# Kernel tuning notes

Measured on AMD Instinct MI355X. Metric: run time of the kernel, lower is better.

The kernel has to match this reference:

```python
import jax, jax.numpy as jnp
import numpy as np

B, S, H, NH = 2, 2048, 2048, 16
HD = H // NH


def setup_inputs() -> dict:
    key = jax.random.key(0)
    ks = jax.random.split(key, 9)
    s = 1.0 / np.sqrt(H)
    return {
        "hidden_state": jax.random.normal(ks[0], (B, S, H), dtype=jnp.float32),
        "Wq": jax.random.normal(ks[1], (H, H), dtype=jnp.float32) * s,
        "bq": jnp.zeros((H,), dtype=jnp.float32),
        "Wk": jax.random.normal(ks[2], (H, H), dtype=jnp.float32) * s,
        "bk": jnp.zeros((H,), dtype=jnp.float32),
        "Wv": jax.random.normal(ks[3], (H, H), dtype=jnp.float32) * s,
        "bv": jnp.zeros((H,), dtype=jnp.float32),
        "Wo": jax.random.normal(ks[4], (H, H), dtype=jnp.float32) * s,
        "bo": jnp.zeros((H,), dtype=jnp.float32),
    }


def _split_heads(x):
    # [B,S,H] -> [B,NH,S,HD]
    b, s, _ = x.shape
    return x.reshape(b, s, NH, HD).transpose(0, 2, 1, 3)


def reference(hidden_state, Wq, bq, Wk, bk, Wv, bv, Wo, bo):
    q = _split_heads(hidden_state @ Wq.T + bq)
    k = _split_heads(hidden_state @ Wk.T + bk)
    v = _split_heads(hidden_state @ Wv.T + bv)
    scale = 1.0 / jnp.sqrt(jnp.array(HD, dtype=q.dtype))
    scores = jnp.einsum("bhqd,bhkd->bhqk", q, k) * scale
    attn = jax.nn.softmax(scores, axis=-1)
    out = jnp.einsum("bhqk,bhkd->bhqd", attn, v)  # [B,NH,S,HD]
    out = out.transpose(0, 2, 1, 3).reshape(hidden_state.shape[0], -1, H)
    return out @ Wo.T + bo
```

## Files before the change

### kernel.cpp

```cpp
#include <hip/hip_runtime.h>
#include <hip/hip_bf16.h>
#include <stdint.h>

#define B_ 2
#define S_ 2048
#define H_ 2048
#define NH_ 16
#define HD_ 128
#define M_ (B_*S_)

typedef __attribute__((ext_vector_type(8))) short short8_t;
typedef __attribute__((ext_vector_type(4))) float floatx4;
typedef __attribute__((ext_vector_type(16))) float floatx16;

__device__ __forceinline__ short f2bf(float f) {
  union { float f; uint32_t u; } x; x.f = f;
  const uint32_t u = x.u;
  return (short)((u + 0x7FFFu + ((u >> 16) & 1u)) >> 16);
}

__device__ __forceinline__ float exp2_fast(float x) {
  float r;
  asm("v_exp_f32 %0, %1" : "=v"(r) : "v"(x));
  return r;
}

__device__ __forceinline__ void gload_lds16(const void* g, void* l) {
  __builtin_amdgcn_global_load_lds(
      (const __attribute__((address_space(1))) void*)g,
      (__attribute__((address_space(3))) void*)l, 16, 0, 0);
}

__global__ __launch_bounds__(256)
void cast_all(const float* __restrict__ h,  const float* __restrict__ wq,
              const float* __restrict__ wk, const float* __restrict__ wv,
              const float* __restrict__ wo,
              short* __restrict__ hB,  short* __restrict__ wqB,
              short* __restrict__ wkB, short* __restrict__ wvB,
              short* __restrict__ woB) {
  const int blk = blockIdx.x;
  const float* src; short* dst; int off;
  if      (blk <  4096) { src = h;  dst = hB;  off = blk; }
  else if (blk <  6144) { src = wq; dst = wqB; off = blk - 4096; }
  else if (blk <  8192) { src = wk; dst = wkB; off = blk - 6144; }
  else if (blk < 10240) { src = wv; dst = wvB; off = blk - 8192; }
  else                  { src = wo; dst = woB; off = blk - 10240; }
  const int i = (off * 256 + threadIdx.x) * 8;
  typedef __attribute__((ext_vector_type(4))) float f4;
  const f4 a = *(const f4*)(src + i);
  const f4 b = *(const f4*)(src + i + 4);
  short8_t o;
  o[0] = f2bf(a[0]); o[1] = f2bf(a[1]); o[2] = f2bf(a[2]); o[3] = f2bf(a[3]);
  o[4] = f2bf(b[0]); o[5] = f2bf(b[1]); o[6] = f2bf(b[2]); o[7] = f2bf(b[3]);
  *(short8_t*)(dst + i) = o;
}

__device__ __forceinline__
void gemm256(const short* __restrict__ A, const short* __restrict__ Bm,
             const float* __restrict__ bias, short* __restrict__ C,
             const int m0, const int n0, const int N, const int K) {
  extern __shared__ short lds[];
  const int tid = threadIdx.x;
  const int w  = tid >> 6, ln = tid & 63;
  const int lr = ln >> 4,  lc = ln & 15;
  const int wm = (w >> 2) << 7;
  const int wn = (w & 3) << 6;

  const int srow = ln >> 3;
  const int schk = (ln & 7) ^ srow;
  const short* aS = A  + (size_t)(m0 + w * 16 + srow) * K + schk * 8;
  const short* bS = Bm + (size_t)(n0 + w * 16 + srow) * K + schk * 8;
  const int dA = (w * 16) * 64;

#define SA_LO(u_) do { const int q_ = ((u_) & 1) * 32768;                    \
    gload_lds16(aS + (u_) * 64,                    &lds[q_ + dA]);           \
    gload_lds16(aS + (u_) * 64 + (size_t)8 * K,    &lds[q_ + dA + 512]); } while (0)
#define SA_HI(u_) do { const int q_ = ((u_) & 1) * 32768;                    \
    gload_lds16(aS + (u_) * 64 + (size_t)128 * K,  &lds[q_ + 8192 + dA]);    \
    gload_lds16(aS + (u_) * 64 + (size_t)136 * K,  &lds[q_ + 8192 + dA + 512]); } while (0)
#define SB_LO(u_) do { const int q_ = ((u_) & 1) * 32768;                    \
    gload_lds16(bS + (u_) * 64,                    &lds[q_ + 16384 + dA]);   \
    gload_lds16(bS + (u_) * 64 + (size_t)8 * K,    &lds[q_ + 16384 + dA + 512]); } while (0)
#define SB_HI(u_) do { const int q_ = ((u_) & 1) * 32768;                    \
    gload_lds16(bS + (u_) * 64 + (size_t)128 * K,  &lds[q_ + 24576 + dA]);   \
    gload_lds16(bS + (u_) * 64 + (size_t)136 * K,  &lds[q_ + 24576 + dA + 512]); } while (0)

  const int fsw = (lc & 7) << 3;
  const int k0o = (lr * 8) ^ fsw;
  const int k1o = (32 + lr * 8) ^ fsw;
  const int aro = (wm + lc) * 64;
  const int bro = 16384 + (wn + lc) * 64;

  floatx4 acc[8][4] = {};
  short8_t af[8], b0f[4], b1f[4];

  const int NT = K >> 6;
  SA_LO(0); SA_HI(0); SB_LO(0); SB_HI(0);
  SA_LO(1); SB_LO(1); SB_HI(1);
  asm volatile("s_waitcnt vmcnt(6)" ::: "memory");
  __builtin_amdgcn_s_barrier();

  for (int u = 0; u < NT; ++u) {
    const int Bb = (u & 1) * 32768;
#pragma unroll
    for (int mf = 0; mf < 4; ++mf) {
      af[mf * 2]     = *(const short8_t*)&lds[Bb + aro + mf * 1024 + k0o];
      af[mf * 2 + 1] = *(const short8_t*)&lds[Bb + aro + mf * 1024 + k1o];
    }
#pragma unroll
    for (int nf = 0; nf < 2; ++nf) {
      b0f[nf * 2]     = *(const short8_t*)&lds[Bb + bro + nf * 1024 + k0o];
      b0f[nf * 2 + 1] = *(const short8_t*)&lds[Bb + bro + nf * 1024 + k1o];
    }
    if (u + 1 < NT) SA_HI(u + 1);
    __builtin_amdgcn_sched_barrier(0);
    __builtin_amdgcn_s_barrier();
    asm volatile("s_waitcnt lgkmcnt(0)" ::: "memory");
    __builtin_amdgcn_sched_barrier(0);
    __builtin_amdgcn_s_setprio(1);
#pragma unroll
    for (int mf = 0; mf < 4; ++mf)
#pragma unroll
      for (int nf = 0; nf < 2; ++nf) {
        acc[mf][nf] = __builtin_amdgcn_mfma_f32_16x16x32_bf16(af[mf*2],   b0f[nf*2],   acc[mf][nf], 0, 0, 0);
        acc[mf][nf] = __builtin_amdgcn_mfma_f32_16x16x32_bf16(af[mf*2+1], b0f[nf*2+1], acc[mf][nf], 0, 0, 0);
      }
    __builtin_amdgcn_s_setprio(0);
#pragma unroll
    for (int nf = 0; nf < 2; ++nf) {
      b1f[nf * 2]     = *(const short8_t*)&lds[Bb + bro + (nf + 2) * 1024 + k0o];
      b1f[nf * 2 + 1] = *(const short8_t*)&lds[Bb + bro + (nf + 2) * 1024 + k1o];
    }
    __builtin_amdgcn_sched_barrier(0);
    __builtin_amdgcn_s_barrier();
    asm volatile("s_waitcnt lgkmcnt(0)" ::: "memory");
    __builtin_amdgcn_sched_barrier(0);
    __builtin_amdgcn_s_setprio(1);
#pragma unroll
    for (int mf = 0; mf < 4; ++mf)
#pragma unroll
      for (int nf = 0; nf < 2; ++nf) {
        acc[mf][nf+2] = __builtin_amdgcn_mfma_f32_16x16x32_bf16(af[mf*2],   b1f[nf*2],   acc[mf][nf+2], 0, 0, 0);
        acc[mf][nf+2] = __builtin_amdgcn_mfma_f32_16x16x32_bf16(af[mf*2+1], b1f[nf*2+1], acc[mf][nf+2], 0, 0, 0);
      }
    __builtin_amdgcn_s_setprio(0);
#pragma unroll
    for (int mf = 0; mf < 4; ++mf) {
      af[mf * 2]     = *(const short8_t*)&lds[Bb + aro + 4096 + mf * 1024 + k0o];
      af[mf * 2 + 1] = *(const short8_t*)&lds[Bb + aro + 4096 + mf * 1024 + k1o];
    }
    if (u + 2 < NT) SA_LO(u + 2);
    __builtin_amdgcn_sched_barrier(0);
    __builtin_amdgcn_s_barrier();
    asm volatile("s_waitcnt lgkmcnt(0)" ::: "memory");
    __builtin_amdgcn_sched_barrier(0);
    __builtin_amdgcn_s_setprio(1);
#pragma unroll
    for (int mf = 0; mf < 4; ++mf)
#pragma unroll
      for (int nf = 0; nf < 2; ++nf) {
        acc[4+mf][nf+2] = __builtin_amdgcn_mfma_f32_16x16x32_bf16(af[mf*2],   b1f[nf*2],   acc[4+mf][nf+2], 0, 0, 0);
        acc[4+mf][nf+2] = __builtin_amdgcn_mfma_f32_16x16x32_bf16(af[mf*2+1], b1f[nf*2+1], acc[4+mf][nf+2], 0, 0, 0);
      }
    __builtin_amdgcn_s_setprio(0);
    if (u + 2 < NT) {
      SB_LO(u + 2); SB_HI(u + 2);
      asm volatile("s_waitcnt vmcnt(6)" ::: "memory");
    } else {
      asm volatile("s_waitcnt vmcnt(0)" ::: "memory");
    }
    __builtin_amdgcn_sched_barrier(0);
    __builtin_amdgcn_s_barrier();
    asm volatile("s_waitcnt lgkmcnt(0)" ::: "memory");
    __builtin_amdgcn_sched_barrier(0);
    __builtin_amdgcn_s_setprio(1);
#pragma unroll
    for (int mf = 0; mf < 4; ++mf)
#pragma unroll
      for (int nf = 0; nf < 2; ++nf) {
        acc[4+mf][nf] = __builtin_amdgcn_mfma_f32_16x16x32_bf16(af[mf*2],   b0f[nf*2],   acc[4+mf][nf], 0, 0, 0);
        acc[4+mf][nf] = __builtin_amdgcn_mfma_f32_16x16x32_bf16(af[mf*2+1], b0f[nf*2+1], acc[4+mf][nf], 0, 0, 0);
      }
    __builtin_amdgcn_s_setprio(0);
  }
#undef SA_LO
#undef SA_HI
#undef SB_LO
#undef SB_HI

#pragma unroll
  for (int mf = 0; mf < 8; ++mf) {
#pragma unroll
    for (int nf = 0; nf < 4; ++nf) {
      const int col = n0 + wn + nf * 16 + lc;
      const float bv = bias[col];
#pragma unroll
      for (int r = 0; r < 4; ++r) {
        const int row = m0 + wm + mf * 16 + lr * 4 + r;
        C[(size_t)row * N + col] = f2bf(acc[mf][nf][r] + bv);
      }
    }
  }
}

__global__ __launch_bounds__(512, 2)
void gemm_qkv(const short* __restrict__ A,
              const short* __restrict__ W0, const short* __restrict__ W1, const short* __restrict__ W2,
              const float* __restrict__ b0, const float* __restrict__ b1, const float* __restrict__ b2,
              short* __restrict__ C0, short* __restrict__ C1, short* __restrict__ C2) {
  const int f   = blockIdx.y * 24 + blockIdx.x;
  const int xcd = f & 7, s = f >> 3;
  const int xt  = xcd * 3 + (s >> 4);
  const int mt  = s & 15;
  const int sel = xt >> 3, nt = xt & 7;
  const short* Bm   = sel == 0 ? W0 : (sel == 1 ? W1 : W2);
  const float* bias = sel == 0 ? b0 : (sel == 1 ? b1 : b2);
  short* C          = sel == 0 ? C0 : (sel == 1 ? C1 : C2);
  gemm256(A, Bm, bias, C, mt * 256, nt * 256, H_, H_);
}

template<int MODE>
__device__ __forceinline__
void gemm_body256(const short* __restrict__ A, const short* __restrict__ Bm,
                  const float* __restrict__ bias, void* __restrict__ C,
                  const int m0, const int n0, const int N, const int K) {
  extern __shared__ short lds[];
  short* As = lds;
  short* Bs = lds + 32768;

  const int tid = threadIdx.x;
  const int w  = tid >> 6, ln = tid & 63;
  const int lr = ln >> 4,  lc = ln & 15;
  const int wm = (w >> 1) << 6;
  const int wn = (w & 1) << 6;

  const int srr = ln >> 2;
  const int sgc = (ln & 3) ^ ((ln >> 3) & 3);

  const short* aSrc0 = A  + (size_t)(m0 + (w * 2 + 0) * 16 + srr) * K + sgc * 8;
  const short* aSrc1 = A  + (size_t)(m0 + (w * 2 + 1) * 16 + srr) * K + sgc * 8;
  const short* bSrc  = Bm + (size_t)(n0 +  w * 16          + srr) * K + sgc * 8;

  const int aDst0 = (w * 2 + 0) * 512;
  const int aDst1 = (w * 2 + 1) * 512;
  const int bDst  =  w * 512;

#define STAGE_(t_) do {                                      \
    const int bq_ = (t_) & 3; const int ko_ = (t_) * 32;     \
    gload_lds16(aSrc0 + ko_, &As[bq_ * 8192 + aDst0]);       \
    gload_lds16(aSrc1 + ko_, &As[bq_ * 8192 + aDst1]);       \
    gload_lds16(bSrc  + ko_, &Bs[bq_ * 4096 + bDst]);        \
  } while (0)

  STAGE_(0); STAGE_(1); STAGE_(2);

  floatx4 acc[4][4] = {};
  const int swz = (lr ^ ((lc >> 1) & 3)) << 3;
  const int aro = (wm + lc) * 32 + swz;
  const int bro = (wn + lc) * 32 + swz;

  asm volatile("s_waitcnt vmcnt(6)" ::: "memory");
  __builtin_amdgcn_s_barrier();

  const int NT = K >> 5;
  for (int t = 0; t < NT; ++t) {
    const int cb = t & 3;
    short8_t af[4], bfr[4];
#pragma unroll
    for (int i = 0; i < 4; ++i)
      af[i] = *(const short8_t*)&As[cb * 8192 + aro + i * 512];
#pragma unroll
    for (int j = 0; j < 4; ++j)
      bfr[j] = *(const short8_t*)&Bs[cb * 4096 + bro + j * 512];

    if (t + 3 < NT) STAGE_(t + 3);

    __builtin_amdgcn_s_barrier();
    asm volatile("s_waitcnt lgkmcnt(0)" ::: "memory");
    __builtin_amdgcn_sched_barrier(0);
    __builtin_amdgcn_s_setprio(1);
#pragma unroll
    for (int i = 0; i < 4; ++i)
#pragma unroll
      for (int j = 0; j < 4; ++j)
        acc[i][j] = __builtin_amdgcn_mfma_f32_16x16x32_bf16(af[i], bfr[j], acc[i][j], 0, 0, 0);
    __builtin_amdgcn_s_setprio(0);
    __builtin_amdgcn_sched_barrier(0);
    if (t < NT - 3)       asm volatile("s_waitcnt vmcnt(6)" ::: "memory");
    else if (t == NT - 3) asm volatile("s_waitcnt vmcnt(3)" ::: "memory");
    else if (t == NT - 2) asm volatile("s_waitcnt vmcnt(0)" ::: "memory");
    __builtin_amdgcn_s_barrier();
  }
#undef STAGE_

#pragma unroll
  for (int i = 0; i < 4; ++i) {
#pragma unroll
    for (int j = 0; j < 4; ++j) {
      const int col = n0 + wn + j * 16 + lc;
      const float bv = bias[col];
#pragma unroll
      for (int r = 0; r < 4; ++r) {
        const int row = m0 + wm + i * 16 + lr * 4 + r;
        const float v = acc[i][j][r] + bv;
        if (MODE == 1) ((float*)C)[(size_t)row * N + col] = v;
        else           ((short*)C)[(size_t)row * N + col] = f2bf(v);
      }
    }
  }
}

__global__ __launch_bounds__(512, 2)
void gemm_out(const short* __restrict__ A, const short* __restrict__ Bm,
              const float* __restrict__ bias, float* __restrict__ C) {
  gemm_body256<1>(A, Bm, bias, C, blockIdx.y * 256, blockIdx.x * 128, H_, H_);
}

__global__ __launch_bounds__(256)
void arrange_v(const short* __restrict__ V, short* __restrict__ Vt) {
  __shared__ short T[64][72];
  const int b = blockIdx.z;
  const int s0 = blockIdx.x * 64, c0 = blockIdx.y * 64;
  const int t = threadIdx.x;
  const int r = t >> 3, c8 = (t & 7) * 8;
  const int kt = s0 >> 6;
#pragma unroll
  for (int p = 0; p < 2; ++p) {
    const int row = p * 32 + r;
    *(short8_t*)&T[row][c8] =
        *(const short8_t*)&V[(size_t)(b * S_ + s0 + row) * H_ + c0 + c8];
  }
  __syncthreads();
#pragma unroll
  for (int p = 0; p < 2; ++p) {
    const int row = p * 32 + r;
    const int gcol = c0 + row;
    const int hh = gcol >> 7, d = gcol & 127;
    short8_t o;
#pragma unroll
    for (int j = 0; j < 8; ++j) o[j] = T[c8 + j][row];
    const int chunk = (c8 >> 3) ^ (d & 7);
    *(short8_t*)&Vt[((((size_t)(b * 16 + hh) * 32 + kt) * 128 + d) << 6) + chunk * 8] = o;
  }
}

__global__ __launch_bounds__(256, 2)
void attention(const short* __restrict__ Q, const short* __restrict__ Kg,
               const short* __restrict__ Vt, short* __restrict__ O) {
  __shared__ short Ks[2][64 * 128];
  __shared__ short Vs[2][128 * 64];
  __shared__ float invLds[128];

  const int tid = threadIdx.x;
  const int wv = tid >> 6, ln = tid & 63;
  const int l32 = ln & 31, lh = ln >> 5;
  const int bh = blockIdx.y, b = bh >> 4, h = bh & 15;
  const int qw = blockIdx.x * 128 + wv * 32;

  const short* Qp  = Q  + ((size_t)(b * S_ + qw)) * H_ + h * HD_;
  const short* VtB = Vt + (size_t)bh * (S_ * HD_) + (size_t)wv * 2048 + ln * 8;

  const short* kp[4];
#pragma unroll
  for (int j = 0; j < 4; ++j) {
    const int key = wv * 16 + j * 4 + (ln >> 4);
    const int sc = (ln & 15) ^ (key & 7);
    kp[j] = Kg + (size_t)(b * S_ + key) * H_ + h * HD_ + sc * 8;
  }

  short8_t qf[8];
#pragma unroll
  for (int ksq = 0; ksq < 8; ++ksq)
    qf[ksq] = *(const short8_t*)&Qp[(size_t)l32 * H_ + ksq * 16 + lh * 8];

  floatx16 oacc[4] = {};
  float lsum = 0.f;
  const float csc = 0.08838834764831845f * 1.4426950408889634f;

#pragma unroll
  for (int j = 0; j < 4; ++j)
    gload_lds16(kp[j], &Ks[0][(wv * 16 + j * 4) * 128]);
#pragma unroll
  for (int j = 0; j < 4; ++j)
    gload_lds16(VtB + j * 512, &Vs[0][wv * 2048 + j * 512]);

  for (int kt = 0; kt < S_ / 64; ++kt) {
    const int cur = kt & 1;
    __syncthreads();

    if (kt + 1 < S_ / 64) {
      const size_t kadv = (size_t)(kt + 1) * 64 * H_;
#pragma unroll
      for (int j = 0; j < 4; ++j)
        gload_lds16(kp[j] + kadv, &Ks[cur ^ 1][(wv * 16 + j * 4) * 128]);
#pragma unroll
      for (int j = 0; j < 4; ++j)
        gload_lds16(VtB + (size_t)(kt + 1) * 8192 + j * 512, &Vs[cur ^ 1][wv * 2048 + j * 512]);
    }

    floatx16 sacc[2] = {};
    __builtin_amdgcn_s_setprio(1);
#pragma unroll
    for (int kh = 0; kh < 2; ++kh) {
      const int key = kh * 32 + l32;
      const int swk = (key & 7) * 8;
#pragma unroll
      for (int ksq = 0; ksq < 8; ++ksq) {
        const short8_t kf =
            *(const short8_t*)&Ks[cur][key * 128 + (((ksq * 2 + lh) * 8) ^ swk)];
        sacc[kh] = __builtin_amdgcn_mfma_f32_32x32x16_bf16(kf, qf[ksq], sacc[kh], 0, 0, 0);
      }
    }
    __builtin_amdgcn_s_setprio(0);

    int pfr[4][4];
#pragma unroll
    for (int kh = 0; kh < 2; ++kh) {
      uint32_t P[8];
#pragma unroll
      for (int i = 0; i < 8; ++i) {
        const uint32_t u0 = __float_as_uint(exp2_fast(sacc[kh][2 * i] * csc));
        const uint32_t u1 = __float_as_uint(exp2_fast(sacc[kh][2 * i + 1] * csc));
        lsum += __uint_as_float(u0 & 0xffff0000u) + __uint_as_float(u1 & 0xffff0000u);
        P[i] = (u0 >> 16) | (u1 & 0xffff0000u);
      }
#pragma unroll
      for (int t = 0; t < 2; ++t)
#pragma unroll
        for (int j = 0; j < 2; ++j) {
          const int a = (int)P[t * 4 + j], bb = (int)P[t * 4 + j + 2];
          const int as = __shfl_xor(a, 32), bs = __shfl_xor(bb, 32);
          pfr[kh * 2 + t][j]     = lh ? bs : a;
          pfr[kh * 2 + t][j + 2] = lh ? bb : as;
        }
    }

    __builtin_amdgcn_s_setprio(1);
#pragma unroll
    for (int kf = 0; kf < 4; ++kf) {
      union { int i[4]; short8_t s; } pu;
#pragma unroll
      for (int j = 0; j < 4; ++j) pu.i[j] = pfr[kf][j];
#pragma unroll
      for (int dt = 0; dt < 4; ++dt) {
        const int d = dt * 32 + l32;
        const short8_t vf =
            *(const short8_t*)&Vs[cur][d * 64 + (((kf * 2 + lh) * 8) ^ ((d & 7) * 8))];
        oacc[dt] = __builtin_amdgcn_mfma_f32_32x32x16_bf16(pu.s, vf, oacc[dt], 0, 0, 0);
      }
    }
    __builtin_amdgcn_s_setprio(0);
  }

  const float l = lsum + __shfl_xor(lsum, 32);
  invLds[wv * 32 + l32] = 1.0f / l;
  float inv[16];
#pragma unroll
  for (int r = 0; r < 16; ++r)
    inv[r] = invLds[wv * 32 + (r & 3) + 8 * (r >> 2) + 4 * lh];
  short* Op = O + ((size_t)(b * S_ + qw)) * H_ + h * HD_;
#pragma unroll
  for (int dt = 0; dt < 4; ++dt)
#pragma unroll
    for (int r = 0; r < 16; ++r) {
      const int rowl = (r & 3) + 8 * (r >> 2) + 4 * lh;
      Op[(size_t)rowl * H_ + dt * 32 + l32] = f2bf(oacc[dt][r] * inv[r]);
    }
}

extern "C" void kernel_launch(void* const* d_in, const int* in_sizes, int n_in,
                              void* d_out, int out_size, void* d_ws, size_t ws_size,
                              hipStream_t stream) {
  const float* hidden = (const float*)d_in[0];
  const float* Wq = (const float*)d_in[1];
  const float* bq = (const float*)d_in[2];
  const float* Wk = (const float*)d_in[3];
  const float* bk = (const float*)d_in[4];
  const float* Wv = (const float*)d_in[5];
  const float* bv = (const float*)d_in[6];
  const float* Wo = (const float*)d_in[7];
  const float* bo = (const float*)d_in[8];
  float* out = (float*)d_out;

  char* ws = (char*)d_ws;
  short* hB  = (short*)(ws);
  short* WqB = (short*)(ws + (16u << 20));
  short* WkB = (short*)(ws + (24u << 20));
  short* WvB = (short*)(ws + (32u << 20));
  short* WoB = (short*)(ws + (40u << 20));
  short* Qb  = (short*)(ws + (48u << 20));
  short* Kb  = (short*)(ws + (64u << 20));
  short* Vb  = (short*)(ws + (80u << 20));
  short* Vtb = (short*)(ws + (96u << 20));
  short* Ob  = (short*)(ws + (112u << 20));

  constexpr int QKV_LDS = 2 * 2 * 16384 * 2;
  constexpr int OUT_LDS = (4 * 8192 + 4 * 4096) * 2;
  static int lds_set = 0;
  if (!lds_set) {
    lds_set = 1;
    (void)hipFuncSetAttribute((const void*)gemm_qkv,
        hipFuncAttributeMaxDynamicSharedMemorySize, QKV_LDS);
    (void)hipFuncSetAttribute((const void*)gemm_out,
        hipFuncAttributeMaxDynamicSharedMemorySize, OUT_LDS);
  }

  cast_all<<<12288, 256, 0, stream>>>(hidden, Wq, Wk, Wv, Wo, hB, WqB, WkB, WvB, WoB);

  gemm_qkv<<<dim3(24, 16), 512, QKV_LDS, stream>>>(hB, WqB, WkB, WvB, bq, bk, bv, Qb, Kb, Vb);

  arrange_v<<<dim3(S_ / 64, H_ / 64, B_), 256, 0, stream>>>(Vb, Vtb);

  attention<<<dim3(S_ / 128, B_ * NH_), 256, 0, stream>>>(Qb, Kb, Vtb, Ob);

  gemm_out<<<dim3(16, 16), 512, OUT_LDS, stream>>>(Ob, WoB, bo, out);
}
```

Baseline: 394.0 us.

## Fuse V transpose into QKV GEMM epilogue and restructure out-GEMM barriers

The QKV GEMM now writes the V projection straight into the swizzled transposed tile layout that attention consumes, using 4-element vector stores. This removes the separate arrange_v kernel and its extra read and write of the V tensor. Separately, the output GEMM loop moves its vmcnt wait and barrier ahead of the MFMA block, going from two barriers per k-step to one. The cost is scattered epilogue stores for V and a changed wait/barrier schedule in the out GEMM, which could alter how loads overlap with compute.

Result: faster. 382.7 us (-2.9%).

```diff
diff --git a/kernel.cpp b/kernel.cpp
--- a/kernel.cpp
+++ b/kernel.cpp
@@ -10,6 +10,7 @@
 #define M_ (B_*S_)
 
 typedef __attribute__((ext_vector_type(8))) short short8_t;
+typedef __attribute__((ext_vector_type(4))) short short4_t;
 typedef __attribute__((ext_vector_type(4))) float floatx4;
 typedef __attribute__((ext_vector_type(16))) float floatx16;
 
@@ -58,7 +59,8 @@
 __device__ __forceinline__
 void gemm256(const short* __restrict__ A, const short* __restrict__ Bm,
              const float* __restrict__ bias, short* __restrict__ C,
-             const int m0, const int n0, const int N, const int K) {
+             const int m0, const int n0, const int N, const int K,
+             const int vmode) {
   extern __shared__ short lds[];
   const int tid = threadIdx.x;
   const int w  = tid >> 6, ln = tid & 63;
@@ -194,10 +196,25 @@
     for (int nf = 0; nf < 4; ++nf) {
       const int col = n0 + wn + nf * 16 + lc;
       const float bv = bias[col];
-#pragma unroll
-      for (int r = 0; r < 4; ++r) {
-        const int row = m0 + wm + mf * 16 + lr * 4 + r;
-        C[(size_t)row * N + col] = f2bf(acc[mf][nf][r] + bv);
+      if (!vmode) {
+#pragma unroll
+        for (int r = 0; r < 4; ++r) {
+          const int row = m0 + wm + mf * 16 + lr * 4 + r;
+          C[(size_t)row * N + col] = f2bf(acc[mf][nf][r] + bv);
+        }
+      } else {
+        const int row0 = m0 + wm + mf * 16 + lr * 4;
+        const int bb = row0 >> 11, s = row0 & (S_ - 1);
+        const int hh = col >> 7,  dd = col & 127;
+        const size_t base =
+            ((((size_t)(bb * 16 + hh) * 32 + (s >> 6)) * 128 + dd) << 6)
+            + (((((s >> 3) & 7) << 3) ^ ((dd & 7) << 3)) + (s & 7));
+        short4_t v4;
+        v4[0] = f2bf(acc[mf][nf][0] + bv);
+        v4[1] = f2bf(acc[mf][nf][1] + bv);
+        v4[2] = f2bf(acc[mf][nf][2] + bv);
+        v4[3] = f2bf(acc[mf][nf][3] + bv);
+        *(short4_t*)&C[base] = v4;
       }
     }
   }
@@ -216,7 +233,7 @@
   const short* Bm   = sel == 0 ? W0 : (sel == 1 ? W1 : W2);
   const float* bias = sel == 0 ? b0 : (sel == 1 ? b1 : b2);
   short* C          = sel == 0 ? C0 : (sel == 1 ? C1 : C2);
-  gemm256(A, Bm, bias, C, mt * 256, nt * 256, H_, H_);
+  gemm256(A, Bm, bias, C, mt * 256, nt * 256, H_, H_, sel == 2 ? 1 : 0);
 }
 
 template<int MODE>
@@ -275,6 +292,10 @@
 
     if (t + 3 < NT) STAGE_(t + 3);
 
+    if (t < NT - 3)       asm volatile("s_waitcnt vmcnt(6)" ::: "memory");
+    else if (t == NT - 3) asm volatile("s_waitcnt vmcnt(3)" ::: "memory");
+    else                  asm volatile("s_waitcnt vmcnt(0)" ::: "memory");
+    __builtin_amdgcn_sched_barrier(0);
     __builtin_amdgcn_s_barrier();
     asm volatile("s_waitcnt lgkmcnt(0)" ::: "memory");
     __builtin_amdgcn_sched_barrier(0);
@@ -285,11 +306,6 @@
       for (int j = 0; j < 4; ++j)
         acc[i][j] = __builtin_amdgcn_mfma_f32_16x16x32_bf16(af[i], bfr[j], acc[i][j], 0, 0, 0);
     __builtin_amdgcn_s_setprio(0);
-    __builtin_amdgcn_sched_barrier(0);
-    if (t < NT - 3)       asm volatile("s_waitcnt vmcnt(6)" ::: "memory");
-    else if (t == NT - 3) asm volatile("s_waitcnt vmcnt(3)" ::: "memory");
-    else if (t == NT - 2) asm volatile("s_waitcnt vmcnt(0)" ::: "memory");
-    __builtin_amdgcn_s_barrier();
   }
 #undef STAGE_
 
@@ -314,34 +330,6 @@
 void gemm_out(const short* __restrict__ A, const short* __restrict__ Bm,
               const float* __restrict__ bias, float* __restrict__ C) {
   gemm_body256<1>(A, Bm, bias, C, blockIdx.y * 256, blockIdx.x * 128, H_, H_);
-}
-
-__global__ __launch_bounds__(256)
-void arrange_v(const short* __restrict__ V, short* __restrict__ Vt) {
-  __shared__ short T[64][72];
-  const int b = blockIdx.z;
-  const int s0 = blockIdx.x * 64, c0 = blockIdx.y * 64;
-  const int t = threadIdx.x;
-  const int r = t >> 3, c8 = (t & 7) * 8;
-  const int kt = s0 >> 6;
-#pragma unroll
-  for (int p = 0; p < 2; ++p) {
-    const int row = p * 32 + r;
-    *(short8_t*)&T[row][c8] =
-        *(const short8_t*)&V[(size_t)(b * S_ + s0 + row) * H_ + c0 + c8];
-  }
-  __syncthreads();
-#pragma unroll
-  for (int p = 0; p < 2; ++p) {
-    const int row = p * 32 + r;
-    const int gcol = c0 + row;
-    const int hh = gcol >> 7, d = gcol & 127;
-    short8_t o;
-#pragma unroll
-    for (int j = 0; j < 8; ++j) o[j] = T[c8 + j][row];
-    const int chunk = (c8 >> 3) ^ (d & 7);
-    *(short8_t*)&Vt[((((size_t)(b * 16 + hh) * 32 + kt) * 128 + d) << 6) + chunk * 8] = o;
-  }
 }
 
 __global__ __launch_bounds__(256, 2)
@@ -490,7 +478,6 @@
   short* WoB = (short*)(ws + (40u << 20));
   short* Qb  = (short*)(ws + (48u << 20));
   short* Kb  = (short*)(ws + (64u << 20));
-  short* Vb  = (short*)(ws + (80u << 20));
   short* Vtb = (short*)(ws + (96u << 20));
   short* Ob  = (short*)(ws + (112u << 20));
 
@@ -507,9 +494,7 @@
 
   cast_all<<<12288, 256, 0, stream>>>(hidden, Wq, Wk, Wv, Wo, hB, WqB, WkB, WvB, WoB);
 
-  gemm_qkv<<<dim3(24, 16), 512, QKV_LDS, stream>>>(hB, WqB, WkB, WvB, bq, bk, bv, Qb, Kb, Vb);
-
-  arrange_v<<<dim3(S_ / 64, H_ / 64, B_), 256, 0, stream>>>(Vb, Vtb);
+  gemm_qkv<<<dim3(24, 16), 512, QKV_LDS, stream>>>(hB, WqB, WkB, WvB, bq, bk, bv, Qb, Kb, Vtb);
 
   attention<<<dim3(S_ / 128, B_ * NH_), 256, 0, stream>>>(Qb, Kb, Vtb, Ob);
 
```
